# Kernel optimization log

Measured on AMD Instinct MI355X. Metric: run time of the kernel, lower is better.

Reference implementation:

```python
import jax, jax.numpy as jnp
import numpy as np

H, C = 4, 64          # heads, head_dim; H*C == hidden_channels == 256
HID = H * C
NT, NC = 50000, 10000
E_TT, E_CT = 400000, 200000
FT, FC = 128, 64


def _gat(xs, xd, att_s, att_d, bias, src, dst, num_dst):
    """PyG GATConv message passing. xs/xd: projected feats [Ns,H,C]/[Nd,H,C]."""
    a = (xs * att_s).sum(-1)[src] + (xd * att_d).sum(-1)[dst]      # [E,H]
    a = jax.nn.leaky_relu(a, 0.2)
    m = jax.ops.segment_max(a, dst, num_segments=num_dst)          # [Nd,H]
    m = jnp.where(jnp.isfinite(m), m, 0.0)
    ex = jnp.exp(a - m[dst])                                       # [E,H]
    den = jax.ops.segment_sum(ex, dst, num_segments=num_dst)       # [Nd,H]
    msg = jax.ops.segment_sum(ex[:, :, None] * xs[src], dst, num_segments=num_dst)  # [Nd,H,C]
    out = msg / jnp.maximum(den, 1e-16)[:, :, None]
    return out.reshape(num_dst, HID) + bias


def setup_inputs() -> dict:
    key = jax.random.key(0)
    ks = jax.random.split(key, 24)

    def glorot(k, shape):
        fan_in = shape[0] if len(shape) > 1 else shape[-1]
        return jax.random.normal(k, shape, jnp.float32) / np.sqrt(fan_in)

    inp = {
        'x_target': jax.random.normal(ks[0], (NT, FT), jnp.float32),
        'x_context': jax.random.normal(ks[1], (NC, FC), jnp.float32),
        'ei_tt': jax.random.randint(ks[2], (2, E_TT), 0, NT, jnp.int32),
        'ei_ct_src': jax.random.randint(ks[3], (E_CT,), 0, NC, jnp.int32),
        'ei_ct_dst': jax.random.randint(ks[4], (E_CT,), 0, NT, jnp.int32),
        # HeteroDictLinear pretransform
        'Wt': glorot(ks[5], (FT, HID)), 'bt': jnp.zeros((HID,), jnp.float32),
        'Wc': glorot(ks[6], (FC, HID)), 'bc': jnp.zeros((HID,), jnp.float32),
        # DirGATConv: src->dst GATConv
        'W_s2d': glorot(ks[7], (HID, HID)),
        'as_s2d': glorot(ks[8], (H, C)), 'ad_s2d': glorot(ks[9], (H, C)),
        'b_s2d': jnp.zeros((HID,), jnp.float32),
        # DirGATConv: dst->src GATConv
        'W_d2s': glorot(ks[10], (HID, HID)),
        'as_d2s': glorot(ks[11], (H, C)), 'ad_d2s': glorot(ks[12], (H, C)),
        'b_d2s': jnp.zeros((HID,), jnp.float32),
        # bipartite context->target GATConv
        'W_ct_src': glorot(ks[13], (HID, HID)), 'W_ct_dst': glorot(ks[14], (HID, HID)),
        'as_ct': glorot(ks[15], (H, C)), 'ad_ct': glorot(ks[16], (H, C)),
        'b_ct': jnp.zeros((HID,), jnp.float32),
        # final Linear(hidden, hidden)
        'W_out': glorot(ks[17], (HID, HID)), 'b_out': jnp.zeros((HID,), jnp.float32),
    }
    return inp


def reference(x_target, x_context, ei_tt, ei_ct_src, ei_ct_dst,
              Wt, bt, Wc, bc,
              W_s2d, as_s2d, ad_s2d, b_s2d,
              W_d2s, as_d2s, ad_d2s, b_d2s,
              W_ct_src, W_ct_dst, as_ct, ad_ct, b_ct,
              W_out, b_out):
    nt = x_target.shape[0]
    # HeteroDictLinear pretransform + relu
    ht = jax.nn.relu(x_target @ Wt + bt)      # [NT, HID]
    hc = jax.nn.relu(x_context @ Wc + bc)     # [NC, HID]

    # homogeneous target-target edges with self-loops (PyG GATConv default)
    loops = jnp.arange(nt, dtype=ei_tt.dtype)
    src = jnp.concatenate([ei_tt[0], loops])
    dst = jnp.concatenate([ei_tt[1], loops])

    # DirGATConv: (1-alpha)*conv(x, ei) + alpha*conv(x, ei^T), alpha=0.5
    p1 = (ht @ W_s2d).reshape(nt, H, C)
    out_s2d = _gat(p1, p1, as_s2d, ad_s2d, b_s2d, src, dst, nt)
    p2 = (ht @ W_d2s).reshape(nt, H, C)
    out_d2s = _gat(p2, p2, as_d2s, ad_d2s, b_d2s, dst, src, nt)
    out_tt = 0.5 * out_s2d + 0.5 * out_d2s

    # bipartite context->target GATConv (no self-loops)
    ps = (hc @ W_ct_src).reshape(hc.shape[0], H, C)
    pd = (ht @ W_ct_dst).reshape(nt, H, C)
    out_ct = _gat(ps, pd, as_ct, ad_ct, b_ct, ei_ct_src, ei_ct_dst, nt)

    # HeteroConv aggr='mean', then skip connection + relu, then final Linear
    x = (out_tt + out_ct) * 0.5
    x = jax.nn.relu(x + ht)
    return x @ W_out + b_out
```

## Files before the change

kernel.cpp:

```cpp
#include <hip/hip_runtime.h>
#include <hip/hip_bf16.h>
#include <cstdint>
#include <cstddef>


#define LRELU_SLOPE 0.2f
#define CAP 64
#define NRANGE 8

typedef __attribute__((ext_vector_type(8))) short short8;
typedef __attribute__((ext_vector_type(4))) float floatx4;

__device__ __forceinline__ float bf2f(ushort u) {
    union { unsigned int u32; float f; } v; v.u32 = ((unsigned int)u) << 16; return v.f;
}
__device__ __forceinline__ ushort f2bf(float x) {
    union { float f; unsigned int u; } v; v.f = x;
    unsigned int r = (v.u + 0x7FFFu + ((v.u >> 16) & 1u)) >> 16;
    return (ushort)r;
}

__global__ __launch_bounds__(256) void prep_all(
    const float* __restrict__ xt, ushort* __restrict__ xtb,
    const float* __restrict__ xc, ushort* __restrict__ xcb,
    const float* __restrict__ Wt,  ushort* __restrict__ WtT,
    const float* __restrict__ Wc,  ushort* __restrict__ WcT,
    const float* __restrict__ W1,  ushort* __restrict__ W1T,
    const float* __restrict__ W2,  ushort* __restrict__ W2T,
    const float* __restrict__ W3,  ushort* __restrict__ W3T,
    const float* __restrict__ W4,  ushort* __restrict__ W4T,
    int s0, int s1, int s2, int s3, int s4, int s5, int s6, int s7)
{
    const int idx = blockIdx.x * blockDim.x + threadIdx.x;
    if (idx < s0) {
        float4 v = ((const float4*)xt)[idx];
        ushort4 o;
        o.x = f2bf(v.x); o.y = f2bf(v.y); o.z = f2bf(v.z); o.w = f2bf(v.w);
        ((ushort4*)xtb)[idx] = o;
    } else if (idx < s1) {
        const int i = idx - s0;
        float4 v = ((const float4*)xc)[i];
        ushort4 o;
        o.x = f2bf(v.x); o.y = f2bf(v.y); o.z = f2bf(v.z); o.w = f2bf(v.w);
        ((ushort4*)xcb)[i] = o;
    } else if (idx < s2) {
        const int i = idx - s1, k = i >> 8, n = i & 255;
        WtT[n * 128 + k] = f2bf(Wt[i]);
    } else if (idx < s3) {
        const int i = idx - s2, k = i >> 8, n = i & 255;
        WcT[n * 64 + k] = f2bf(Wc[i]);
    } else if (idx < s4) {
        const int i = idx - s3, k = i >> 8, n = i & 255;
        W1T[n * 256 + k] = f2bf(W1[i]);
    } else if (idx < s5) {
        const int i = idx - s4, k = i >> 8, n = i & 255;
        W2T[n * 256 + k] = f2bf(W2[i]);
    } else if (idx < s6) {
        const int i = idx - s5, k = i >> 8, n = i & 255;
        W3T[n * 256 + k] = f2bf(W3[i]);
    } else if (idx < s7) {
        const int i = idx - s6, k = i >> 8, n = i & 255;
        W4T[n * 256 + k] = f2bf(W4[i]);
    }
}

__device__ __forceinline__ void gemm_core(
    const ushort* __restrict__ A, const ushort* __restrict__ Bt,
    const float* __restrict__ bias, float* __restrict__ Cf,
    ushort* __restrict__ Cb, int M, int K, int do_relu,
    const float* __restrict__ attS, const float* __restrict__ attD,
    float* __restrict__ aSo, float* __restrict__ aDo,
    int row0, int col0)
{
    __shared__ short As[64][40];
    __shared__ short Bs[64][40];
    const int tid  = threadIdx.x;
    const int lr = tid >> 2;
    const int lk = (tid & 3) * 8;
    const int w    = tid >> 6;
    const int lane = tid & 63;
    const int mrow = 16 * w + (lane & 15);
    const int ksel = (lane >> 4) * 8;

    floatx4 acc0 = {0.f,0.f,0.f,0.f}, acc1 = acc0, acc2 = acc0, acc3 = acc0;

    for (int k0 = 0; k0 < K; k0 += 32) {
        short8 av = {0,0,0,0,0,0,0,0};
        if (row0 + lr < M)
            av = *(const short8*)(A + (size_t)(row0 + lr) * K + k0 + lk);
        *(short8*)&As[lr][lk] = av;
        *(short8*)&Bs[lr][lk] =
            *(const short8*)(Bt + (size_t)(col0 + lr) * K + k0 + lk);
        __syncthreads();
        short8 af = *(const short8*)&As[mrow][ksel];
        short8 b0 = *(const short8*)&Bs[ 0 + (lane & 15)][ksel];
        short8 b1 = *(const short8*)&Bs[16 + (lane & 15)][ksel];
        short8 b2 = *(const short8*)&Bs[32 + (lane & 15)][ksel];
        short8 b3 = *(const short8*)&Bs[48 + (lane & 15)][ksel];
        acc0 = __builtin_amdgcn_mfma_f32_16x16x32_bf16(af, b0, acc0, 0, 0, 0);
        acc1 = __builtin_amdgcn_mfma_f32_16x16x32_bf16(af, b1, acc1, 0, 0, 0);
        acc2 = __builtin_amdgcn_mfma_f32_16x16x32_bf16(af, b2, acc2, 0, 0, 0);
        acc3 = __builtin_amdgcn_mfma_f32_16x16x32_bf16(af, b3, acc3, 0, 0, 0);
        __syncthreads();
    }

    const int rbase = row0 + 16 * w + (lane >> 4) * 4;
    floatx4 av[4] = {acc0, acc1, acc2, acc3};
#pragma unroll
    for (int c = 0; c < 4; ++c) {
        const int col = col0 + 16 * c + (lane & 15);
        const float bv = bias ? bias[col] : 0.f;
#pragma unroll
        for (int i = 0; i < 4; ++i) {
            const int row = rbase + i;
            if (row < M) {
                float v = av[c][i] + bv;
                if (do_relu) v = fmaxf(v, 0.f);
                const size_t off = (size_t)row * 256 + col;
                if (Cf) Cf[off] = v;
                if (Cb) Cb[off] = f2bf(v);
            }
        }
    }

    if (attS) {
        const int cix = lane & 15;
        float sA[4] = {0.f,0.f,0.f,0.f}, sD[4] = {0.f,0.f,0.f,0.f};
#pragma unroll
        for (int c = 0; c < 4; ++c) {
            const float as_v = attS[col0 + 16 * c + cix];
            const float ad_v = attD ? attD[col0 + 16 * c + cix] : 0.f;
#pragma unroll
            for (int i = 0; i < 4; ++i) {
                sA[i] += av[c][i] * as_v;
                sD[i] += av[c][i] * ad_v;
            }
        }
#pragma unroll
        for (int off = 1; off < 16; off <<= 1) {
#pragma unroll
            for (int i = 0; i < 4; ++i) {
                sA[i] += __shfl_xor(sA[i], off);
                sD[i] += __shfl_xor(sD[i], off);
            }
        }
        if (cix == 0) {
            const int head = col0 >> 6;
#pragma unroll
            for (int i = 0; i < 4; ++i) {
                const int row = rbase + i;
                if (row < M) {
                    aSo[(size_t)row * 4 + head] = sA[i];
                    if (aDo) aDo[(size_t)row * 4 + head] = sD[i];
                }
            }
        }
    }
}

__global__ __launch_bounds__(256) void gemm_bf16(
    const ushort* __restrict__ A, const ushort* __restrict__ Bt,
    const float* __restrict__ bias, float* __restrict__ Cf,
    ushort* __restrict__ Cb, int M, int K, int do_relu)
{
    const int row0 = blockIdx.x * 64;
    if (row0 >= M) return;
    gemm_core(A, Bt, bias, Cf, Cb, M, K, do_relu,
              nullptr, nullptr, nullptr, nullptr, row0, blockIdx.y * 64);
}

__global__ __launch_bounds__(256) void gemm_proj3(
    const ushort* __restrict__ htb, const ushort* __restrict__ hcb,
    const ushort* __restrict__ W1T, const ushort* __restrict__ W2T,
    const ushort* __restrict__ W3T,
    ushort* __restrict__ Pb1, ushort* __restrict__ Pb2, ushort* __restrict__ PSb,
    const float* __restrict__ as1, const float* __restrict__ ad1,
    const float* __restrict__ as2, const float* __restrict__ ad2,
    const float* __restrict__ asc,
    float* __restrict__ aS1, float* __restrict__ aD1,
    float* __restrict__ aS2, float* __restrict__ aD2,
    float* __restrict__ aSc, int NT, int NC)
{
    const int y = blockIdx.y;
    const int row0 = blockIdx.x * 64;
    if (y < 4) {
        if (row0 >= NT) return;
        gemm_core(htb, W1T, nullptr, nullptr, Pb1, NT, 256, 0,
                  as1, ad1, aS1, aD1, row0, y * 64);
    } else if (y < 8) {
        if (row0 >= NT) return;
        gemm_core(htb, W2T, nullptr, nullptr, Pb2, NT, 256, 0,
                  as2, ad2, aS2, aD2, row0, (y - 4) * 64);
    } else {
        if (row0 >= NC) return;
        gemm_core(hcb, W3T, nullptr, nullptr, PSb, NC, 256, 0,
                  asc, nullptr, aSc, nullptr, row0, (y - 8) * 64);
    }
}

__global__ void fold_ct(const float* __restrict__ W, const float* __restrict__ ad,
                        float* __restrict__ wfold)
{
    int idx = blockIdx.x * blockDim.x + threadIdx.x;
    if (idx >= 1024) return;
    int k = idx >> 2, h = idx & 3;
    float s = 0.f;
#pragma unroll 8
    for (int c = 0; c < 64; ++c) s += W[(size_t)k * 256 + h * 64 + c] * ad[h * 64 + c];
    wfold[idx] = s;
}

__global__ __launch_bounds__(256) void alpha_from_fold(
    const ushort* __restrict__ ht, const float* __restrict__ wfold,
    float* __restrict__ aD, int N)
{
    __shared__ float wf[1024];
    const int tid = threadIdx.x;
    *(float4*)&wf[tid * 4] = *(const float4*)&wfold[tid * 4];
    __syncthreads();
    const int idx = blockIdx.x * 256 + tid;
    if (idx >= N * 4) return;
    const int n = idx >> 2, h = idx & 3;
    const ushort* row = ht + (size_t)n * 256;
    float s = 0.f;
#pragma unroll
    for (int k = 0; k < 256; k += 4) {
        ushort4 r4 = *(const ushort4*)(row + k);
        s += bf2f(r4.x) * wf[(k + 0) * 4 + h] + bf2f(r4.y) * wf[(k + 1) * 4 + h]
           + bf2f(r4.z) * wf[(k + 2) * 4 + h] + bf2f(r4.w) * wf[(k + 3) * 4 + h];
    }
    aD[idx] = s;
}

__global__ __launch_bounds__(256) void build_all_buckets(
    const int* __restrict__ tt_src, const int* __restrict__ tt_dst, int E_tt,
    const int* __restrict__ ct_src, const int* __restrict__ ct_dst, int E_ct,
    int RS,
    int* __restrict__ cntA, int* __restrict__ bktA,
    int* __restrict__ cntB, int* __restrict__ bktB,
    int* __restrict__ cntC, int* __restrict__ bktC)
{
    const int bx = (blockIdx.x < 512) ? blockIdx.x : blockIdx.x - 512;
    const int range = bx & (NRANGE - 1);
    const int lo = range * RS, hi = lo + RS;
    const int j  = bx >> 3;
    const int stride = 64 * blockDim.x;
    if (blockIdx.x < 512) {
        for (int e = j * blockDim.x + threadIdx.x; e < E_tt; e += stride) {
            const int s = tt_src[e], d = tt_dst[e];
            if (d >= lo && d < hi) {
                const int pa = atomicAdd(&cntA[d], 1);
                if (pa < CAP) bktA[(size_t)d * CAP + pa] = s;
            }
            if (s >= lo && s < hi) {
                const int pb = atomicAdd(&cntB[s], 1);
                if (pb < CAP) bktB[(size_t)s * CAP + pb] = d;
            }
        }
    } else {
        for (int e = j * blockDim.x + threadIdx.x; e < E_ct; e += stride) {
            const int s = ct_src[e], d = ct_dst[e];
            if (d >= lo && d < hi) {
                const int p = atomicAdd(&cntC[d], 1);
                if (p < CAP) bktC[(size_t)d * CAP + p] = s;
            }
        }
    }
}

__device__ __forceinline__ void gat_phase(
    int n, int h, int c4,
    const int* __restrict__ cnt, const int* __restrict__ bkt,
    const float* __restrict__ aS, const float* __restrict__ aD,
    const ushort* __restrict__ X, const float* __restrict__ bias,
    float scale, int has_self, float4& out)
{
    const float aDn = aD[(size_t)n * 4 + h];
    float4 f = {0.f, 0.f, 0.f, 0.f};
    float den = 0.f;
    if (has_self) {
        float a = aS[(size_t)n * 4 + h] + aDn;
        a = (a >= 0.f) ? a : LRELU_SLOPE * a;
        const float w = __expf(a);
        const ushort4 x = *(const ushort4*)(X + (size_t)n * 256 + c4);
        f.x = w * bf2f(x.x); f.y = w * bf2f(x.y);
        f.z = w * bf2f(x.z); f.w = w * bf2f(x.w);
        den = w;
    }
    const int deg = min(cnt[n], CAP);
    const int* b = bkt + (size_t)n * CAP;
    int i = 0;
    for (; i + 4 <= deg; i += 4) {
        const int s0 = b[i], s1 = b[i + 1], s2 = b[i + 2], s3 = b[i + 3];
        float a0 = aS[(size_t)s0 * 4 + h] + aDn;
        float a1 = aS[(size_t)s1 * 4 + h] + aDn;
        float a2 = aS[(size_t)s2 * 4 + h] + aDn;
        float a3 = aS[(size_t)s3 * 4 + h] + aDn;
        a0 = (a0 >= 0.f) ? a0 : LRELU_SLOPE * a0;
        a1 = (a1 >= 0.f) ? a1 : LRELU_SLOPE * a1;
        a2 = (a2 >= 0.f) ? a2 : LRELU_SLOPE * a2;
        a3 = (a3 >= 0.f) ? a3 : LRELU_SLOPE * a3;
        const float w0 = __expf(a0), w1 = __expf(a1);
        const float w2 = __expf(a2), w3 = __expf(a3);
        const ushort4 x0 = *(const ushort4*)(X + (size_t)s0 * 256 + c4);
        const ushort4 x1 = *(const ushort4*)(X + (size_t)s1 * 256 + c4);
        const ushort4 x2 = *(const ushort4*)(X + (size_t)s2 * 256 + c4);
        const ushort4 x3 = *(const ushort4*)(X + (size_t)s3 * 256 + c4);
        f.x += w0 * bf2f(x0.x) + w1 * bf2f(x1.x) + w2 * bf2f(x2.x) + w3 * bf2f(x3.x);
        f.y += w0 * bf2f(x0.y) + w1 * bf2f(x1.y) + w2 * bf2f(x2.y) + w3 * bf2f(x3.y);
        f.z += w0 * bf2f(x0.z) + w1 * bf2f(x1.z) + w2 * bf2f(x2.z) + w3 * bf2f(x3.z);
        f.w += w0 * bf2f(x0.w) + w1 * bf2f(x1.w) + w2 * bf2f(x2.w) + w3 * bf2f(x3.w);
        den += w0 + w1 + w2 + w3;
    }
    for (; i < deg; ++i) {
        const int s = b[i];
        float a = aS[(size_t)s * 4 + h] + aDn;
        a = (a >= 0.f) ? a : LRELU_SLOPE * a;
        const float w = __expf(a);
        const ushort4 x = *(const ushort4*)(X + (size_t)s * 256 + c4);
        f.x += w * bf2f(x.x); f.y += w * bf2f(x.y);
        f.z += w * bf2f(x.z); f.w += w * bf2f(x.w);
        den += w;
    }
    const float inv = 1.f / fmaxf(den, 1e-16f);
    const float4 bv = *(const float4*)(bias + c4);
    out.x += scale * (f.x * inv + bv.x);
    out.y += scale * (f.y * inv + bv.y);
    out.z += scale * (f.z * inv + bv.z);
    out.w += scale * (f.w * inv + bv.w);
}

__global__ __launch_bounds__(256) void gat_gather_fused(
    const int* __restrict__ cntA, const int* __restrict__ bktA,
    const float* __restrict__ aS1, const float* __restrict__ aD1,
    const ushort* __restrict__ P1, const float* __restrict__ b1,
    const int* __restrict__ cntB, const int* __restrict__ bktB,
    const float* __restrict__ aS2, const float* __restrict__ aD2,
    const ushort* __restrict__ P2, const float* __restrict__ b2,
    const int* __restrict__ cntC, const int* __restrict__ bktC,
    const float* __restrict__ aSc, const float* __restrict__ aDc,
    const ushort* __restrict__ Pc, const float* __restrict__ b3,
    ushort* __restrict__ htb, int N)
{
    const int n = blockIdx.x * 4 + (threadIdx.x >> 6);
    if (n >= N) return;
    const int lane = threadIdx.x & 63;
    const int h  = lane >> 4;
    const int c4 = lane << 2;

    float4 out = {0.f, 0.f, 0.f, 0.f};
    gat_phase(n, h, c4, cntA, bktA, aS1, aD1, P1, b1, 0.25f, 1, out);
    gat_phase(n, h, c4, cntB, bktB, aS2, aD2, P2, b2, 0.25f, 1, out);
    gat_phase(n, h, c4, cntC, bktC, aSc, aDc, Pc, b3, 0.50f, 0, out);

    ushort* hp = htb + (size_t)n * 256 + c4;
    const ushort4 hb = *(const ushort4*)hp;
    ushort4 o;
    o.x = f2bf(fmaxf(out.x + bf2f(hb.x), 0.f));
    o.y = f2bf(fmaxf(out.y + bf2f(hb.y), 0.f));
    o.z = f2bf(fmaxf(out.z + bf2f(hb.z), 0.f));
    o.w = f2bf(fmaxf(out.w + bf2f(hb.w), 0.f));
    *(ushort4*)hp = o;
}

extern "C" void kernel_launch(void* const* d_in, const int* in_sizes, int n_in,
                              void* d_out, int out_size, void* d_ws, size_t ws_size,
                              hipStream_t stream)
{
    const int NT   = in_sizes[0] / 128;
    const int NC   = in_sizes[1] / 64;
    const int E_TT = in_sizes[2] / 2;
    const int E_CT = in_sizes[3];

    const float* x_target = (const float*)d_in[0];
    const float* x_context= (const float*)d_in[1];
    const int*   ei_tt    = (const int*)d_in[2];
    const int*   ei_ct_src= (const int*)d_in[3];
    const int*   ei_ct_dst= (const int*)d_in[4];
    const float* Wt   = (const float*)d_in[5];
    const float* bt   = (const float*)d_in[6];
    const float* Wc   = (const float*)d_in[7];
    const float* bc   = (const float*)d_in[8];
    const float* W_s2d  = (const float*)d_in[9];
    const float* as_s2d = (const float*)d_in[10];
    const float* ad_s2d = (const float*)d_in[11];
    const float* b_s2d  = (const float*)d_in[12];
    const float* W_d2s  = (const float*)d_in[13];
    const float* as_d2s = (const float*)d_in[14];
    const float* ad_d2s = (const float*)d_in[15];
    const float* b_d2s  = (const float*)d_in[16];
    const float* W_ct_src = (const float*)d_in[17];
    const float* W_ct_dst = (const float*)d_in[18];
    const float* as_ct  = (const float*)d_in[19];
    const float* ad_ct  = (const float*)d_in[20];
    const float* b_ct   = (const float*)d_in[21];
    const float* W_out  = (const float*)d_in[22];
    const float* b_out  = (const float*)d_in[23];
    float* out = (float*)d_out;

    const int* tt_src = ei_tt;
    const int* tt_dst = ei_tt + E_TT;

    float* ws = (float*)d_ws;
    size_t o = 0;
    ushort* htb = (ushort*)(ws + o);   o += (size_t)NT * 128;
    ushort* Pb1 = (ushort*)(ws + o);   o += (size_t)NT * 128;
    ushort* Pb2 = (ushort*)(ws + o);   o += (size_t)NT * 128;
    ushort* hcb = (ushort*)(ws + o);   o += (size_t)NC * 128;
    ushort* PSb = (ushort*)(ws + o);   o += (size_t)NC * 128;
    ushort* xtb = (ushort*)(ws + o);   o += (size_t)NT * 64;
    ushort* xcb = (ushort*)(ws + o);   o += (size_t)NC * 32;
    int* bktA = (int*)(ws + o);        o += (size_t)NT * CAP;
    int* bktB = (int*)(ws + o);        o += (size_t)NT * CAP;
    int* bktC = (int*)(ws + o);        o += (size_t)NT * CAP;
    float* aS1 = ws + o;               o += (size_t)NT * 4;
    float* aD1 = ws + o;               o += (size_t)NT * 4;
    float* aS2 = ws + o;               o += (size_t)NT * 4;
    float* aD2 = ws + o;               o += (size_t)NT * 4;
    float* aSc = ws + o;               o += (size_t)NT * 4;
    float* aDc = ws + o;               o += (size_t)NT * 4;
    int*   cntA = (int*)(ws + o);      o += (size_t)NT;
    int*   cntB = (int*)(ws + o);      o += (size_t)NT;
    int*   cntC = (int*)(ws + o);      o += (size_t)NT;
    float* wfold = ws + o;             o += 1024;
    ushort* WtT   = (ushort*)(ws + o); o += 128 * 256 / 2;
    ushort* WcT   = (ushort*)(ws + o); o += 64 * 256 / 2;
    ushort* Ws2dT = (ushort*)(ws + o); o += 256 * 256 / 2;
    ushort* Wd2sT = (ushort*)(ws + o); o += 256 * 256 / 2;
    ushort* WctsT = (ushort*)(ws + o); o += 256 * 256 / 2;
    ushort* WoutT = (ushort*)(ws + o); o += 256 * 256 / 2;
    (void)ws_size; (void)n_in; (void)out_size;

    const dim3 blk(256);
    const int gN4 = (NT * 4 + 255) / 256;
    const int gGat = (NT + 3) / 4;
    const int RS = (NT + NRANGE - 1) / NRANGE;

    hipMemsetAsync(cntA, 0, (size_t)NT * 3 * sizeof(int), stream);

    const int s0 = NT * 32;
    const int s1 = s0 + NC * 16;
    const int s2 = s1 + 128 * 256;
    const int s3 = s2 + 64 * 256;
    const int s4 = s3 + 65536;
    const int s5 = s4 + 65536;
    const int s6 = s5 + 65536;
    const int s7 = s6 + 65536;
    hipLaunchKernelGGL(prep_all, dim3((s7 + 255) / 256), blk, 0, stream,
                       x_target, xtb, x_context, xcb,
                       Wt, WtT, Wc, WcT, W_s2d, Ws2dT, W_d2s, Wd2sT,
                       W_ct_src, WctsT, W_out, WoutT,
                       s0, s1, s2, s3, s4, s5, s6, s7);

    hipLaunchKernelGGL(build_all_buckets, dim3(1024), blk, 0, stream,
                       tt_src, tt_dst, E_TT, ei_ct_src, ei_ct_dst, E_CT, RS,
                       cntA, bktA, cntB, bktB, cntC, bktC);

    hipLaunchKernelGGL(fold_ct, dim3(4), blk, 0, stream, W_ct_dst, ad_ct, wfold);

    hipLaunchKernelGGL(gemm_bf16, dim3((NT + 63) / 64, 4), blk, 0, stream,
                       xtb, WtT, bt, nullptr, htb, NT, 128, 1);
    hipLaunchKernelGGL(gemm_bf16, dim3((NC + 63) / 64, 4), blk, 0, stream,
                       xcb, WcT, bc, nullptr, hcb, NC, 64, 1);

    hipLaunchKernelGGL(gemm_proj3, dim3((NT + 63) / 64, 12), blk, 0, stream,
                       htb, hcb, Ws2dT, Wd2sT, WctsT, Pb1, Pb2, PSb,
                       as_s2d, ad_s2d, as_d2s, ad_d2s, as_ct,
                       aS1, aD1, aS2, aD2, aSc, NT, NC);

    hipLaunchKernelGGL(alpha_from_fold, dim3(gN4), blk, 0, stream,
                       htb, wfold, aDc, NT);

    hipLaunchKernelGGL(gat_gather_fused, dim3(gGat), blk, 0, stream,
                       cntA, bktA, aS1, aD1, Pb1, b_s2d,
                       cntB, bktB, aS2, aD2, Pb2, b_d2s,
                       cntC, bktC, aSc, aDc, PSb, b_ct,
                       htb, NT);

    hipLaunchKernelGGL(gemm_bf16, dim3((NT + 63) / 64, 4), blk, 0, stream,
                       htb, WoutT, b_out, out, nullptr, NT, 256, 0);
}
```

Before: 405.3 us.

## Use 128-row GEMM tiles and fuse small kernels into fewer launches

The GEMM core tile grows from 64x64 to 128x64, so each wave computes two 16-row MFMA strips and reuses each B fragment twice. The fold_ct computation moves into prep_all, the two pretransform GEMMs merge into one gemm_pre2 launch, and alpha_from_fold becomes an extra y-slice of gemm_proj3. This cuts kernel launches and raises arithmetic intensity per loaded B tile. In exchange there are fewer blocks, and gemm_proj3 now has a wider grid (gxA x 13) whose GEMM slices mostly exit early.

```diff
diff --git a/kernel.cpp b/kernel.cpp
--- a/kernel.cpp
+++ b/kernel.cpp
@@ -29,7 +29,9 @@
     const float* __restrict__ W2,  ushort* __restrict__ W2T,
     const float* __restrict__ W3,  ushort* __restrict__ W3T,
     const float* __restrict__ W4,  ushort* __restrict__ W4T,
-    int s0, int s1, int s2, int s3, int s4, int s5, int s6, int s7)
+    const float* __restrict__ Wcd, const float* __restrict__ adc,
+    float* __restrict__ wfold,
+    int s0, int s1, int s2, int s3, int s4, int s5, int s6, int s7, int s8)
 {
     const int idx = blockIdx.x * blockDim.x + threadIdx.x;
     if (idx < s0) {
@@ -61,6 +63,13 @@
     } else if (idx < s7) {
         const int i = idx - s6, k = i >> 8, n = i & 255;
         W4T[n * 256 + k] = f2bf(W4[i]);
+    } else if (idx < s8) {
+        const int i = idx - s7, k = i >> 2, h = i & 3;
+        float s = 0.f;
+#pragma unroll 8
+        for (int c = 0; c < 64; ++c)
+            s += Wcd[(size_t)k * 256 + h * 64 + c] * adc[h * 64 + c];
+        wfold[i] = s;
     }
 }
 
@@ -72,86 +81,108 @@
     float* __restrict__ aSo, float* __restrict__ aDo,
     int row0, int col0)
 {
-    __shared__ short As[64][40];
+    __shared__ short As[128][40];
     __shared__ short Bs[64][40];
     const int tid  = threadIdx.x;
-    const int lr = tid >> 2;
-    const int lk = (tid & 3) * 8;
+    const int ra = tid >> 1;
+    const int ka = (tid & 1) * 16;
+    const int rb = tid >> 2;
+    const int kb = (tid & 3) * 8;
     const int w    = tid >> 6;
     const int lane = tid & 63;
-    const int mrow = 16 * w + (lane & 15);
+    const int cix  = lane & 15;
     const int ksel = (lane >> 4) * 8;
 
-    floatx4 acc0 = {0.f,0.f,0.f,0.f}, acc1 = acc0, acc2 = acc0, acc3 = acc0;
+    floatx4 acc[2][4];
+#pragma unroll
+    for (int r = 0; r < 2; ++r)
+#pragma unroll
+        for (int c = 0; c < 4; ++c) acc[r][c] = (floatx4){0.f, 0.f, 0.f, 0.f};
 
     for (int k0 = 0; k0 < K; k0 += 32) {
-        short8 av = {0,0,0,0,0,0,0,0};
-        if (row0 + lr < M)
-            av = *(const short8*)(A + (size_t)(row0 + lr) * K + k0 + lk);
-        *(short8*)&As[lr][lk] = av;
-        *(short8*)&Bs[lr][lk] =
-            *(const short8*)(Bt + (size_t)(col0 + lr) * K + k0 + lk);
+        short8 a0 = {0,0,0,0,0,0,0,0}, a1 = a0;
+        if (row0 + ra < M) {
+            const ushort* ap = A + (size_t)(row0 + ra) * K + k0 + ka;
+            a0 = *(const short8*)ap;
+            a1 = *(const short8*)(ap + 8);
+        }
+        *(short8*)&As[ra][ka]     = a0;
+        *(short8*)&As[ra][ka + 8] = a1;
+        *(short8*)&Bs[rb][kb] =
+            *(const short8*)(Bt + (size_t)(col0 + rb) * K + k0 + kb);
         __syncthreads();
-        short8 af = *(const short8*)&As[mrow][ksel];
-        short8 b0 = *(const short8*)&Bs[ 0 + (lane & 15)][ksel];
-        short8 b1 = *(const short8*)&Bs[16 + (lane & 15)][ksel];
-        short8 b2 = *(const short8*)&Bs[32 + (lane & 15)][ksel];
-        short8 b3 = *(const short8*)&Bs[48 + (lane & 15)][ksel];
-        acc0 = __builtin_amdgcn_mfma_f32_16x16x32_bf16(af, b0, acc0, 0, 0, 0);
-        acc1 = __builtin_amdgcn_mfma_f32_16x16x32_bf16(af, b1, acc1, 0, 0, 0);
-        acc2 = __builtin_amdgcn_mfma_f32_16x16x32_bf16(af, b2, acc2, 0, 0, 0);
-        acc3 = __builtin_amdgcn_mfma_f32_16x16x32_bf16(af, b3, acc3, 0, 0, 0);
+        const short8 af0 = *(const short8*)&As[32 * w + cix][ksel];
+        const short8 af1 = *(const short8*)&As[32 * w + 16 + cix][ksel];
+#pragma unroll
+        for (int c = 0; c < 4; ++c) {
+            const short8 bf = *(const short8*)&Bs[16 * c + cix][ksel];
+            acc[0][c] = __builtin_amdgcn_mfma_f32_16x16x32_bf16(af0, bf, acc[0][c], 0, 0, 0);
+            acc[1][c] = __builtin_amdgcn_mfma_f32_16x16x32_bf16(af1, bf, acc[1][c], 0, 0, 0);
+        }
         __syncthreads();
     }
 
-    const int rbase = row0 + 16 * w + (lane >> 4) * 4;
-    floatx4 av[4] = {acc0, acc1, acc2, acc3};
-#pragma unroll
-    for (int c = 0; c < 4; ++c) {
-        const int col = col0 + 16 * c + (lane & 15);
-        const float bv = bias ? bias[col] : 0.f;
-#pragma unroll
-        for (int i = 0; i < 4; ++i) {
-            const int row = rbase + i;
-            if (row < M) {
-                float v = av[c][i] + bv;
-                if (do_relu) v = fmaxf(v, 0.f);
-                const size_t off = (size_t)row * 256 + col;
-                if (Cf) Cf[off] = v;
-                if (Cb) Cb[off] = f2bf(v);
+#pragma unroll
+    for (int r = 0; r < 2; ++r) {
+        const int rbase = row0 + 32 * w + 16 * r + (lane >> 4) * 4;
+#pragma unroll
+        for (int c = 0; c < 4; ++c) {
+            const int col = col0 + 16 * c + cix;
+            const float bv = bias ? bias[col] : 0.f;
+#pragma unroll
+            for (int i = 0; i < 4; ++i) {
+                const int row = rbase + i;
+                if (row < M) {
+                    float v = acc[r][c][i] + bv;
+                    if (do_relu) v = fmaxf(v, 0.f);
+                    const size_t off = (size_t)row * 256 + col;
+                    if (Cf) Cf[off] = v;
+                    if (Cb) Cb[off] = f2bf(v);
+                }
             }
         }
     }
 
     if (attS) {
-        const int cix = lane & 15;
-        float sA[4] = {0.f,0.f,0.f,0.f}, sD[4] = {0.f,0.f,0.f,0.f};
+        float sA[2][4], sD[2][4];
+#pragma unroll
+        for (int r = 0; r < 2; ++r)
+#pragma unroll
+            for (int i = 0; i < 4; ++i) { sA[r][i] = 0.f; sD[r][i] = 0.f; }
 #pragma unroll
         for (int c = 0; c < 4; ++c) {
             const float as_v = attS[col0 + 16 * c + cix];
             const float ad_v = attD ? attD[col0 + 16 * c + cix] : 0.f;
 #pragma unroll
-            for (int i = 0; i < 4; ++i) {
-                sA[i] += av[c][i] * as_v;
-                sD[i] += av[c][i] * ad_v;
-            }
+            for (int r = 0; r < 2; ++r)
+#pragma unroll
+                for (int i = 0; i < 4; ++i) {
+                    sA[r][i] += acc[r][c][i] * as_v;
+                    sD[r][i] += acc[r][c][i] * ad_v;
+                }
         }
 #pragma unroll
         for (int off = 1; off < 16; off <<= 1) {
 #pragma unroll
-            for (int i = 0; i < 4; ++i) {
-                sA[i] += __shfl_xor(sA[i], off);
-                sD[i] += __shfl_xor(sD[i], off);
-            }
+            for (int r = 0; r < 2; ++r)
+#pragma unroll
+                for (int i = 0; i < 4; ++i) {
+                    sA[r][i] += __shfl_xor(sA[r][i], off);
+                    sD[r][i] += __shfl_xor(sD[r][i], off);
+                }
         }
         if (cix == 0) {
             const int head = col0 >> 6;
 #pragma unroll
-            for (int i = 0; i < 4; ++i) {
-                const int row = rbase + i;
-                if (row < M) {
-                    aSo[(size_t)row * 4 + head] = sA[i];
-                    if (aDo) aDo[(size_t)row * 4 + head] = sD[i];
+            for (int r = 0; r < 2; ++r) {
+                const int rbase = row0 + 32 * w + 16 * r + (lane >> 4) * 4;
+#pragma unroll
+                for (int i = 0; i < 4; ++i) {
+                    const int row = rbase + i;
+                    if (row < M) {
+                        aSo[(size_t)row * 4 + head] = sA[r][i];
+                        if (aDo) aDo[(size_t)row * 4 + head] = sD[r][i];
+                    }
                 }
             }
         }
@@ -163,10 +194,29 @@
     const float* __restrict__ bias, float* __restrict__ Cf,
     ushort* __restrict__ Cb, int M, int K, int do_relu)
 {
-    const int row0 = blockIdx.x * 64;
+    const int row0 = blockIdx.x * 128;
     if (row0 >= M) return;
     gemm_core(A, Bt, bias, Cf, Cb, M, K, do_relu,
               nullptr, nullptr, nullptr, nullptr, row0, blockIdx.y * 64);
+}
+
+__global__ __launch_bounds__(256) void gemm_pre2(
+    const ushort* __restrict__ xtb, const ushort* __restrict__ WtT,
+    const float* __restrict__ bt, ushort* __restrict__ htb, int NT,
+    const ushort* __restrict__ xcb, const ushort* __restrict__ WcT,
+    const float* __restrict__ bc, ushort* __restrict__ hcb, int NC)
+{
+    const int y = blockIdx.y;
+    const int row0 = blockIdx.x * 128;
+    if (y < 4) {
+        if (row0 >= NT) return;
+        gemm_core(xtb, WtT, bt, nullptr, htb, NT, 128, 1,
+                  nullptr, nullptr, nullptr, nullptr, row0, y * 64);
+    } else {
+        if (row0 >= NC) return;
+        gemm_core(xcb, WcT, bc, nullptr, hcb, NC, 64, 1,
+                  nullptr, nullptr, nullptr, nullptr, row0, (y - 4) * 64);
+    }
 }
 
 __global__ __launch_bounds__(256) void gemm_proj3(
@@ -179,10 +229,31 @@
     const float* __restrict__ asc,
     float* __restrict__ aS1, float* __restrict__ aD1,
     float* __restrict__ aS2, float* __restrict__ aD2,
-    float* __restrict__ aSc, int NT, int NC)
+    float* __restrict__ aSc,
+    const float* __restrict__ wfold, float* __restrict__ aDc,
+    int NT, int NC)
 {
     const int y = blockIdx.y;
-    const int row0 = blockIdx.x * 64;
+    if (y == 12) {
+        __shared__ float wf[1024];
+        const int tid = threadIdx.x;
+        *(float4*)&wf[tid * 4] = *(const float4*)&wfold[tid * 4];
+        __syncthreads();
+        const int idx = blockIdx.x * 256 + tid;
+        if (idx >= NT * 4) return;
+        const int n = idx >> 2, h = idx & 3;
+        const ushort* row = htb + (size_t)n * 256;
+        float s = 0.f;
+#pragma unroll
+        for (int k = 0; k < 256; k += 4) {
+            ushort4 r4 = *(const ushort4*)(row + k);
+            s += bf2f(r4.x) * wf[(k + 0) * 4 + h] + bf2f(r4.y) * wf[(k + 1) * 4 + h]
+               + bf2f(r4.z) * wf[(k + 2) * 4 + h] + bf2f(r4.w) * wf[(k + 3) * 4 + h];
+        }
+        aDc[idx] = s;
+        return;
+    }
+    const int row0 = blockIdx.x * 128;
     if (y < 4) {
         if (row0 >= NT) return;
         gemm_core(htb, W1T, nullptr, nullptr, Pb1, NT, 256, 0,
@@ -196,40 +267,6 @@
         gemm_core(hcb, W3T, nullptr, nullptr, PSb, NC, 256, 0,
                   asc, nullptr, aSc, nullptr, row0, (y - 8) * 64);
     }
-}
-
-__global__ void fold_ct(const float* __restrict__ W, const float* __restrict__ ad,
-                        float* __restrict__ wfold)
-{
-    int idx = blockIdx.x * blockDim.x + threadIdx.x;
-    if (idx >= 1024) return;
-    int k = idx >> 2, h = idx & 3;
-    float s = 0.f;
-#pragma unroll 8
-    for (int c = 0; c < 64; ++c) s += W[(size_t)k * 256 + h * 64 + c] * ad[h * 64 + c];
-    wfold[idx] = s;
-}
-
-__global__ __launch_bounds__(256) void alpha_from_fold(
-    const ushort* __restrict__ ht, const float* __restrict__ wfold,
-    float* __restrict__ aD, int N)
-{
-    __shared__ float wf[1024];
-    const int tid = threadIdx.x;
-    *(float4*)&wf[tid * 4] = *(const float4*)&wfold[tid * 4];
-    __syncthreads();
-    const int idx = blockIdx.x * 256 + tid;
-    if (idx >= N * 4) return;
-    const int n = idx >> 2, h = idx & 3;
-    const ushort* row = ht + (size_t)n * 256;
-    float s = 0.f;
-#pragma unroll
-    for (int k = 0; k < 256; k += 4) {
-        ushort4 r4 = *(const ushort4*)(row + k);
-        s += bf2f(r4.x) * wf[(k + 0) * 4 + h] + bf2f(r4.y) * wf[(k + 1) * 4 + h]
-           + bf2f(r4.z) * wf[(k + 2) * 4 + h] + bf2f(r4.w) * wf[(k + 3) * 4 + h];
-    }
-    aD[idx] = s;
 }
 
 __global__ __launch_bounds__(256) void build_all_buckets(
@@ -432,9 +469,10 @@
     (void)ws_size; (void)n_in; (void)out_size;
 
     const dim3 blk(256);
-    const int gN4 = (NT * 4 + 255) / 256;
     const int gGat = (NT + 3) / 4;
     const int RS = (NT + NRANGE - 1) / NRANGE;
+    const int gxT = (NT + 127) / 128;
+    const int gxA = (NT * 4 + 255) / 256;
 
     hipMemsetAsync(cntA, 0, (size_t)NT * 3 * sizeof(int), stream);
 
@@ -446,30 +484,25 @@
     const int s5 = s4 + 65536;
     const int s6 = s5 + 65536;
     const int s7 = s6 + 65536;
-    hipLaunchKernelGGL(prep_all, dim3((s7 + 255) / 256), blk, 0, stream,
+    const int s8 = s7 + 1024;
+    hipLaunchKernelGGL(prep_all, dim3((s8 + 255) / 256), blk, 0, stream,
                        x_target, xtb, x_context, xcb,
                        Wt, WtT, Wc, WcT, W_s2d, Ws2dT, W_d2s, Wd2sT,
                        W_ct_src, WctsT, W_out, WoutT,
-                       s0, s1, s2, s3, s4, s5, s6, s7);
+                       W_ct_dst, ad_ct, wfold,
+                       s0, s1, s2, s3, s4, s5, s6, s7, s8);
 
     hipLaunchKernelGGL(build_all_buckets, dim3(1024), blk, 0, stream,
                        tt_src, tt_dst, E_TT, ei_ct_src, ei_ct_dst, E_CT, RS,
                        cntA, bktA, cntB, bktB, cntC, bktC);
 
-    hipLaunchKernelGGL(fold_ct, dim3(4), blk, 0, stream, W_ct_dst, ad_ct, wfold);
-
-    hipLaunchKernelGGL(gemm_bf16, dim3((NT + 63) / 64, 4), blk, 0, stream,
-                       xtb, WtT, bt, nullptr, htb, NT, 128, 1);
-    hipLaunchKernelGGL(gemm_bf16, dim3((NC + 63) / 64, 4), blk, 0, stream,
-                       xcb, WcT, bc, nullptr, hcb, NC, 64, 1);
-
-    hipLaunchKernelGGL(gemm_proj3, dim3((NT + 63) / 64, 12), blk, 0, stream,
+    hipLaunchKernelGGL(gemm_pre2, dim3(gxT, 8), blk, 0, stream,
+                       xtb, WtT, bt, htb, NT, xcb, WcT, bc, hcb, NC);
+
+    hipLaunchKernelGGL(gemm_proj3, dim3(gxA, 13), blk, 0, stream,
                        htb, hcb, Ws2dT, Wd2sT, WctsT, Pb1, Pb2, PSb,
                        as_s2d, ad_s2d, as_d2s, ad_d2s, as_ct,
-                       aS1, aD1, aS2, aD2, aSc, NT, NC);
-
-    hipLaunchKernelGGL(alpha_from_fold, dim3(gN4), blk, 0, stream,
-                       htb, wfold, aDc, NT);
+                       aS1, aD1, aS2, aD2, aSc, wfold, aDc, NT, NC);
 
     hipLaunchKernelGGL(gat_gather_fused, dim3(gGat), blk, 0, stream,
                        cntA, bktA, aS1, aD1, Pb1, b_s2d,
@@ -477,6 +510,6 @@
                        cntC, bktC, aSc, aDc, PSb, b_ct,
                        htb, NT);
 
-    hipLaunchKernelGGL(gemm_bf16, dim3((NT + 63) / 64, 4), blk, 0, stream,
+    hipLaunchKernelGGL(gemm_bf16, dim3(gxT, 4), blk, 0, stream,
                        htb, WoutT, b_out, out, nullptr, NT, 256, 0);
 }
```

New measurement: 413.0 us. About the same (+1.9%).
